# Performance work log

Measured on AMD Instinct MI355X. Metric: run time of the kernel, lower is better.

Reference implementation:

```python
import jax, jax.numpy as jnp
import numpy as np

N, E = 50000, 800000
IN_DIM, H_DIM, OUT_DIM, EDGE_DIM, HEADS = 128, 128, 112, 8, 1
NEG_SLOPE = 0.2
BN_EPS = 1e-5


def _gat_layer(x, src, dst, edge_att, W, a_src, a_dst, We, a_edge, bias):
    """PyG GATConv (concat=False, edge_dim used for attention only)."""
    H, C = a_src.shape  # heads, out channels
    xs = (x @ W).reshape(-1, H, C)            # [N,H,C]
    ef = (edge_att @ We).reshape(-1, H, C)    # [E,H,C]
    al_src = jnp.einsum('nhc,hc->nh', xs, a_src)   # [N,H]
    al_dst = jnp.einsum('nhc,hc->nh', xs, a_dst)   # [N,H]
    al_edge = jnp.einsum('ehc,hc->eh', ef, a_edge) # [E,H]
    alpha = al_src[src] + al_dst[dst] + al_edge    # [E,H]
    alpha = jnp.where(alpha > 0, alpha, NEG_SLOPE * alpha)  # leaky_relu(0.2)
    # segment softmax over incoming edges of each dst node
    m = jax.lax.stop_gradient(jax.ops.segment_max(alpha, dst, num_segments=N))
    ex = jnp.exp(alpha - m[dst])
    den = jax.ops.segment_sum(ex, dst, num_segments=N)
    att = ex / den[dst]                       # [E,H]
    msg = xs[src] * att[:, :, None]           # [E,H,C] gather + weight
    out = jax.ops.segment_sum(msg, dst, num_segments=N)  # scatter-add [N,H,C]
    return out.mean(axis=1) + bias            # concat=False -> head mean


def _batchnorm(h, gamma, beta):
    mu = h.mean(axis=0)
    var = h.var(axis=0)
    return gamma * (h - mu) * jax.lax.rsqrt(var + BN_EPS) + beta


def setup_inputs() -> dict:
    key = jax.random.key(0)
    ks = jax.random.split(key, 20)
    s = 0.1
    inp = {
        'x': jax.random.normal(ks[0], (N, IN_DIM), dtype=jnp.float32),
        'edge_index': jax.random.randint(ks[1], (2, E), 0, N, dtype=jnp.int32),
        'edge_att': jax.random.normal(ks[2], (E, EDGE_DIM), dtype=jnp.float32),
        # layer 0: IN_DIM -> H_DIM
        'W0': s * jax.random.normal(ks[3], (IN_DIM, HEADS * H_DIM), dtype=jnp.float32),
        'a_src0': s * jax.random.normal(ks[4], (HEADS, H_DIM), dtype=jnp.float32),
        'a_dst0': s * jax.random.normal(ks[5], (HEADS, H_DIM), dtype=jnp.float32),
        'We0': s * jax.random.normal(ks[6], (EDGE_DIM, HEADS * H_DIM), dtype=jnp.float32),
        'a_edge0': s * jax.random.normal(ks[7], (HEADS, H_DIM), dtype=jnp.float32),
        'b0': jnp.zeros((H_DIM,), dtype=jnp.float32),
        # layer 1: H_DIM -> OUT_DIM
        'W1': s * jax.random.normal(ks[8], (H_DIM, HEADS * OUT_DIM), dtype=jnp.float32),
        'a_src1': s * jax.random.normal(ks[9], (HEADS, OUT_DIM), dtype=jnp.float32),
        'a_dst1': s * jax.random.normal(ks[10], (HEADS, OUT_DIM), dtype=jnp.float32),
        'We1': s * jax.random.normal(ks[11], (EDGE_DIM, HEADS * OUT_DIM), dtype=jnp.float32),
        'a_edge1': s * jax.random.normal(ks[12], (HEADS, OUT_DIM), dtype=jnp.float32),
        'b1': jnp.zeros((OUT_DIM,), dtype=jnp.float32),
        # batchnorms
        'bn_g': jnp.ones((H_DIM,), dtype=jnp.float32),
        'bn_b': jnp.zeros((H_DIM,), dtype=jnp.float32),
        'bnf_g': jnp.ones((OUT_DIM,), dtype=jnp.float32),
        'bnf_b': jnp.zeros((OUT_DIM,), dtype=jnp.float32),
    }
    return inp


def reference(x, edge_index, edge_att,
              W0, a_src0, a_dst0, We0, a_edge0, b0,
              W1, a_src1, a_dst1, We1, a_edge1, b1,
              bn_g, bn_b, bnf_g, bnf_b):
    src, dst = edge_index[0], edge_index[1]
    h = _gat_layer(x, src, dst, edge_att, W0, a_src0, a_dst0, We0, a_edge0, b0)
    h = _batchnorm(h, bn_g, bn_b)
    h = jax.nn.relu(h)
    # dropout is a no-op in eval; omitted for a deterministic reference
    h = _gat_layer(h, src, dst, edge_att, W1, a_src1, a_dst1, We1, a_edge1, b1)
    h = _batchnorm(h, bnf_g, bnf_b)
    return h
```

## Files before the change

kernel.cpp:

```cpp
#include <hip/hip_runtime.h>
#include <math.h>

#define NN 50000
#define NPAD 50048
#define NE 800000
#define SCAN_B 256
#define SCAN_NBLK ((NN + SCAN_B - 1) / SCAN_B)
#define AGG_NBLK 3200

typedef __attribute__((ext_vector_type(8))) short bf16x8;
typedef __attribute__((ext_vector_type(4))) float f32x4;
typedef __attribute__((ext_vector_type(8))) unsigned short u16x8;

__device__ __forceinline__ unsigned short f2bf(float x) {
    unsigned u = __float_as_uint(x);
    u += 0x7fffu + ((u >> 16) & 1);
    return (unsigned short)(u >> 16);
}
__device__ __forceinline__ float bf2f(unsigned short h) {
    return __uint_as_float(((unsigned)h) << 16);
}

template<int LAYER>
__device__ __forceinline__ float edge_ex(uint2 r, float aldv, const float* __restrict__ als)
{
    float ae = bf2f((unsigned short)(LAYER ? (r.y & 0xffffu) : (r.x >> 16)));
    float a = als[r.x & 0xffffu] + aldv + ae;
    a = a > 0.f ? a : 0.2f * a;
    return __expf(a);
}

__global__ void k_init_cvt(int* __restrict__ deg, float* __restrict__ stats,
                           int* __restrict__ hist, int* __restrict__ binCur,
                           const float* __restrict__ We0, const float* __restrict__ ae0,
                           const float* __restrict__ We1, const float* __restrict__ ae1,
                           float* __restrict__ ve,
                           const float* __restrict__ W0, const float* __restrict__ W1,
                           unsigned short* __restrict__ Wth0, unsigned short* __restrict__ Wtl0,
                           unsigned short* __restrict__ Wth1, unsigned short* __restrict__ Wtl1)
{
    int idx = blockIdx.x * 256 + threadIdx.x;
    if (idx < NN) deg[idx] = 0;
    if (idx < 512) stats[idx] = 0.f;
    if (idx < 64) { hist[idx] = 0; binCur[idx] = 0; }
    if (idx < 128 * 128) {
        int k = idx / 128, c = idx % 128;
        float v = W0[idx];
        unsigned short hi = f2bf(v);
        Wth0[c * 128 + k] = hi;
        Wtl0[c * 128 + k] = f2bf(v - bf2f(hi));
    } else if (idx < 128 * 128 + 128 * 112) {
        int i2 = idx - 128 * 128;
        int k = i2 / 112, c = i2 % 112;
        float v = W1[i2];
        unsigned short hi = f2bf(v);
        Wth1[c * 128 + k] = hi;
        Wtl1[c * 128 + k] = f2bf(v - bf2f(hi));
    }
    if (blockIdx.x == gridDim.x - 1) {
        int j = threadIdx.x;
        if (j < 8) {
            float s = 0.f;
            for (int c = 0; c < 128; ++c) s += We0[j * 128 + c] * ae0[c];
            ve[j] = s;
        } else if (j < 16) {
            int jj = j - 8;
            float s = 0.f;
            for (int c = 0; c < 112; ++c) s += We1[jj * 112 + c] * ae1[c];
            ve[8 + jj] = s;
        }
    }
}

__global__ void k_deg(const int* __restrict__ dst, int* __restrict__ deg,
                      int* __restrict__ rank, int E_)
{
    int e = blockIdx.x * blockDim.x + threadIdx.x;
    if (e < E_) rank[e] = atomicAdd(&deg[dst[e]], 1);
}

__global__ void k_scan1(const int* __restrict__ deg, int* __restrict__ partial,
                        int* __restrict__ hist)
{
    __shared__ int sm[SCAN_B];
    __shared__ int lh[64];
    int t = threadIdx.x;
    if (t < 64) lh[t] = 0;
    int idx = blockIdx.x * SCAN_B + t;
    int d = (idx < NN) ? deg[idx] : 0;
    sm[t] = d;
    __syncthreads();
    if (idx < NN) atomicAdd(&lh[63 - (d < 63 ? d : 63)], 1);
    #pragma unroll
    for (int off = SCAN_B / 2; off > 0; off >>= 1) {
        if (t < off) sm[t] += sm[t + off];
        __syncthreads();
    }
    if (t == 0) partial[blockIdx.x] = sm[0];
    if (t < 64 && lh[t]) atomicAdd(&hist[t], lh[t]);
}

__global__ void k_scan3(const int* __restrict__ deg, const int* __restrict__ partial,
                        int* __restrict__ rp, const int* __restrict__ hist,
                        int* __restrict__ binCur, int* __restrict__ ord)
{
    __shared__ int sm[SCAN_B];
    __shared__ int pbase;
    __shared__ int lh[64], lrsv[64], lstart[64];
    int t = threadIdx.x;
    int pv = (t < SCAN_NBLK && t < blockIdx.x) ? partial[t] : 0;
    sm[t] = pv;
    __syncthreads();
    #pragma unroll
    for (int off = SCAN_B / 2; off > 0; off >>= 1) {
        if (t < off) sm[t] += sm[t + off];
        __syncthreads();
    }
    if (t == 0) pbase = sm[0];
    __syncthreads();
    int idx = blockIdx.x * SCAN_B + t;
    int v = (idx < NN) ? deg[idx] : 0;
    sm[t] = v;
    __syncthreads();
    #pragma unroll
    for (int off = 1; off < SCAN_B; off <<= 1) {
        int u = (t >= off) ? sm[t - off] : 0;
        __syncthreads();
        sm[t] += u;
        __syncthreads();
    }
    int excl = pbase + ((t == 0) ? 0 : sm[t - 1]);
    if (idx < NN) rp[idx] = excl;
    if (idx == NN - 1) rp[NN] = excl + v;

    if (t < 64) lh[t] = 0;
    __syncthreads();
    int b = 0, lr = 0;
    if (idx < NN) {
        b = 63 - (v < 63 ? v : 63);
        lr = atomicAdd(&lh[b], 1);
    }
    __syncthreads();
    if (t < 64) {
        lrsv[t] = lh[t] ? atomicAdd(&binCur[t], lh[t]) : 0;
        int s = 0;
        for (int i = 0; i < t; ++i) s += hist[i];
        lstart[t] = s;
    }
    __syncthreads();
    if (idx < NN) ord[lstart[b] + lrsv[b] + lr] = idx;
}

__global__ void k_csr_fill(const int* __restrict__ src, const int* __restrict__ dst,
                           const float* __restrict__ eatt, const float* __restrict__ ve,
                           const int* __restrict__ rp, const int* __restrict__ rank,
                           uint2* __restrict__ pk, int E_)
{
    int i = blockIdx.x * blockDim.x + threadIdx.x;
    int e = i * 2;
    if (e >= E_) return;
    int2 ss = *reinterpret_cast<const int2*>(src + e);
    int2 dd = *reinterpret_cast<const int2*>(dst + e);
    int2 rr = *reinterpret_cast<const int2*>(rank + e);
    const float4* ea = reinterpret_cast<const float4*>(eatt + (size_t)e * 8);
    float4 ea0 = ea[0], ea1 = ea[1], ea2 = ea[2], ea3 = ea[3];

    float a0x = ea0.x * ve[0] + ea0.y * ve[1] + ea0.z * ve[2] + ea0.w * ve[3]
              + ea1.x * ve[4] + ea1.y * ve[5] + ea1.z * ve[6] + ea1.w * ve[7];
    float a1x = ea0.x * ve[8] + ea0.y * ve[9] + ea0.z * ve[10] + ea0.w * ve[11]
              + ea1.x * ve[12] + ea1.y * ve[13] + ea1.z * ve[14] + ea1.w * ve[15];
    float a0y = ea2.x * ve[0] + ea2.y * ve[1] + ea2.z * ve[2] + ea2.w * ve[3]
              + ea3.x * ve[4] + ea3.y * ve[5] + ea3.z * ve[6] + ea3.w * ve[7];
    float a1y = ea2.x * ve[8] + ea2.y * ve[9] + ea2.z * ve[10] + ea2.w * ve[11]
              + ea3.x * ve[12] + ea3.y * ve[13] + ea3.z * ve[14] + ea3.w * ve[15];

    int p0 = rp[dd.x] + rr.x;
    int p1 = rp[dd.y] + rr.y;
    uint2 r0, r1;
    r0.x = (unsigned)ss.x | ((unsigned)f2bf(a0x) << 16);
    r0.y = (unsigned)f2bf(a1x);
    r1.x = (unsigned)ss.y | ((unsigned)f2bf(a0y) << 16);
    r1.y = (unsigned)f2bf(a1y);
    pk[p0] = r0;
    pk[p1] = r1;
}

template<int COLS, bool BN_IN>
__launch_bounds__(256, 2)
__global__ void k_gemm_mfma(const float* __restrict__ A,
                            const unsigned short* __restrict__ Wth,
                            const unsigned short* __restrict__ Wtl,
                            unsigned short* __restrict__ out,
                            const float* __restrict__ a_src, const float* __restrict__ a_dst,
                            float* __restrict__ als, float* __restrict__ ald,
                            const float* __restrict__ bsum, const float* __restrict__ bsq,
                            const float* __restrict__ gamma, const float* __restrict__ beta)
{
    constexpr int NT = COLS / 16;
    __shared__ unsigned short sBh[COLS * 128];
    __shared__ unsigned short sBl[COLS * 128];
    __shared__ float scN[128], shN[128];

    int wv = threadIdx.x >> 6;
    int lane = threadIdx.x & 63;
    int r0 = blockIdx.x * 64 + wv * 16;
    int m = lane & 15;
    int quad = lane >> 4;
    int arow = r0 + m;
    int rc = (arow < NN) ? arow : NN - 1;
    const float* pa = A + (size_t)rc * 128 + quad * 8;

    float4 av[8];
    #pragma unroll
    for (int ks = 0; ks < 4; ++ks) {
        av[2 * ks]     = *reinterpret_cast<const float4*>(pa + ks * 32);
        av[2 * ks + 1] = *reinterpret_cast<const float4*>(pa + ks * 32 + 4);
    }

    constexpr int CH = COLS * 128 * 2 / 16;
    for (int i = threadIdx.x; i < CH; i += 256) {
        unsigned o = (unsigned)i * 16u;
        unsigned d = o ^ (((o >> 8) & 7u) << 4);
        *reinterpret_cast<uint4*>(reinterpret_cast<char*>(sBh) + d) =
            *reinterpret_cast<const uint4*>(reinterpret_cast<const char*>(Wth) + o);
        *reinterpret_cast<uint4*>(reinterpret_cast<char*>(sBl) + d) =
            *reinterpret_cast<const uint4*>(reinterpret_cast<const char*>(Wtl) + o);
    }
    if (BN_IN) {
        if (threadIdx.x < 128) {
            int k = threadIdx.x;
            float invn = 1.0f / (float)NN;
            float mean = bsum[k] * invn;
            float var  = bsq[k] * invn - mean * mean;
            float sc = gamma[k] * rsqrtf(var + 1e-5f);
            scN[k] = sc;
            shN[k] = beta[k] - mean * sc;
        }
    }
    __syncthreads();

    f32x4 acc[NT];
    #pragma unroll
    for (int t = 0; t < NT; ++t) acc[t] = f32x4{0.f, 0.f, 0.f, 0.f};

    unsigned swz = ((unsigned)(m & 7)) << 4;

    #pragma unroll
    for (int ks = 0; ks < 4; ++ks) {
        float4 v0 = av[2 * ks], v1 = av[2 * ks + 1];
        float vv[8] = {v0.x, v0.y, v0.z, v0.w, v1.x, v1.y, v1.z, v1.w};
        int kb = ks * 32 + quad * 8;
        bf16x8 ah, al;
        #pragma unroll
        for (int jj = 0; jj < 8; ++jj) {
            float f = vv[jj];
            if (BN_IN) f = fmaxf(f * scN[kb + jj] + shN[kb + jj], 0.f);
            unsigned short hi = f2bf(f);
            ah[jj] = (short)hi;
            al[jj] = (short)f2bf(f - bf2f(hi));
        }
        #pragma unroll
        for (int t = 0; t < NT; ++t) {
            int c = t * 16 + m;
            unsigned b = ((unsigned)c * 256u + (unsigned)ks * 64u + (unsigned)quad * 16u) ^ swz;
            bf16x8 bh = *reinterpret_cast<const bf16x8*>(reinterpret_cast<const char*>(sBh) + b);
            bf16x8 bl = *reinterpret_cast<const bf16x8*>(reinterpret_cast<const char*>(sBl) + b);
            acc[t] = __builtin_amdgcn_mfma_f32_16x16x32_bf16(ah, bh, acc[t], 0, 0, 0);
            acc[t] = __builtin_amdgcn_mfma_f32_16x16x32_bf16(al, bh, acc[t], 0, 0, 0);
            acc[t] = __builtin_amdgcn_mfma_f32_16x16x32_bf16(ah, bl, acc[t], 0, 0, 0);
        }
    }

    float p[4] = {0.f, 0.f, 0.f, 0.f}, q[4] = {0.f, 0.f, 0.f, 0.f};
    #pragma unroll
    for (int t = 0; t < NT; ++t) {
        int c = t * 16 + m;
        float asv = a_src[c], adv = a_dst[c];
        #pragma unroll
        for (int rI = 0; rI < 4; ++rI) {
            float v = acc[t][rI];
            int row = r0 + quad * 4 + rI;
            if (row < NN) out[(size_t)row * COLS + c] = f2bf(v);
            p[rI] += v * asv;
            q[rI] += v * adv;
        }
    }
    #pragma unroll
    for (int rI = 0; rI < 4; ++rI) {
        #pragma unroll
        for (int off = 1; off <= 8; off <<= 1) {
            p[rI] += __shfl_xor(p[rI], off);
            q[rI] += __shfl_xor(q[rI], off);
        }
    }
    if (m == 0) {
        #pragma unroll
        for (int rI = 0; rI < 4; ++rI) {
            int row = r0 + quad * 4 + rI;
            if (row < NN) { als[row] = p[rI]; ald[row] = q[rI]; }
        }
    }
}

template<int COLS, int LAYER>
__global__ void k_aggregate(const int* __restrict__ rp, const int* __restrict__ ord,
                            const uint2* __restrict__ pk,
                            const float* __restrict__ als, const float* __restrict__ ald,
                            const unsigned short* __restrict__ xs, float* __restrict__ out,
                            float* __restrict__ psum, float* __restrict__ psq)
{
    __shared__ float sS[16 * 128], sQ[16 * 128];
    int ql = threadIdx.x & 15;
    int wq = threadIdx.x >> 4;
    int col = ql * 8;
    bool act = (col < COLS);
    int qid = blockIdx.x * 16 + wq;
    float bs[8] = {0.f,0.f,0.f,0.f,0.f,0.f,0.f,0.f};
    float bq[8] = {0.f,0.f,0.f,0.f,0.f,0.f,0.f,0.f};

    if (qid < NN) {
        int w = ord[qid];
        int beg = rp[w], end = rp[w + 1];
        float aldv = ald[w];
        float acc[8] = {0.f,0.f,0.f,0.f,0.f,0.f,0.f,0.f};
        float den = 0.f;
        int j = beg;
        for (; j + 8 <= end; j += 8) {
            uint2 r0 = pk[j],     r1 = pk[j + 1], r2 = pk[j + 2], r3 = pk[j + 3];
            uint2 r4 = pk[j + 4], r5 = pk[j + 5], r6 = pk[j + 6], r7 = pk[j + 7];
            float e0 = edge_ex<LAYER>(r0, aldv, als), e1 = edge_ex<LAYER>(r1, aldv, als);
            float e2 = edge_ex<LAYER>(r2, aldv, als), e3 = edge_ex<LAYER>(r3, aldv, als);
            float e4 = edge_ex<LAYER>(r4, aldv, als), e5 = edge_ex<LAYER>(r5, aldv, als);
            float e6 = edge_ex<LAYER>(r6, aldv, als), e7 = edge_ex<LAYER>(r7, aldv, als);
            den += ((e0 + e1) + (e2 + e3)) + ((e4 + e5) + (e6 + e7));
            if (act) {
                u16x8 u0 = *reinterpret_cast<const u16x8*>(xs + (size_t)(r0.x & 0xffffu) * COLS + col);
                u16x8 u1 = *reinterpret_cast<const u16x8*>(xs + (size_t)(r1.x & 0xffffu) * COLS + col);
                u16x8 u2 = *reinterpret_cast<const u16x8*>(xs + (size_t)(r2.x & 0xffffu) * COLS + col);
                u16x8 u3 = *reinterpret_cast<const u16x8*>(xs + (size_t)(r3.x & 0xffffu) * COLS + col);
                u16x8 u4 = *reinterpret_cast<const u16x8*>(xs + (size_t)(r4.x & 0xffffu) * COLS + col);
                u16x8 u5 = *reinterpret_cast<const u16x8*>(xs + (size_t)(r5.x & 0xffffu) * COLS + col);
                u16x8 u6 = *reinterpret_cast<const u16x8*>(xs + (size_t)(r6.x & 0xffffu) * COLS + col);
                u16x8 u7 = *reinterpret_cast<const u16x8*>(xs + (size_t)(r7.x & 0xffffu) * COLS + col);
                #pragma unroll
                for (int k = 0; k < 8; ++k)
                    acc[k] += (((e0 * bf2f(u0[k]) + e1 * bf2f(u1[k]))
                              + (e2 * bf2f(u2[k]) + e3 * bf2f(u3[k])))
                             + ((e4 * bf2f(u4[k]) + e5 * bf2f(u5[k]))
                              + (e6 * bf2f(u6[k]) + e7 * bf2f(u7[k]))));
            }
        }
        if (j < end) {
            bool v1 = j + 1 < end, v2 = j + 2 < end, v3 = j + 3 < end;
            bool v4 = j + 4 < end, v5 = j + 5 < end, v6 = j + 6 < end;
            uint2 r0 = pk[j];
            uint2 r1 = v1 ? pk[j + 1] : uint2{0u, 0u};
            uint2 r2 = v2 ? pk[j + 2] : uint2{0u, 0u};
            uint2 r3 = v3 ? pk[j + 3] : uint2{0u, 0u};
            uint2 r4 = v4 ? pk[j + 4] : uint2{0u, 0u};
            uint2 r5 = v5 ? pk[j + 5] : uint2{0u, 0u};
            uint2 r6 = v6 ? pk[j + 6] : uint2{0u, 0u};
            float e0 = edge_ex<LAYER>(r0, aldv, als);
            float e1 = v1 ? edge_ex<LAYER>(r1, aldv, als) : 0.f;
            float e2 = v2 ? edge_ex<LAYER>(r2, aldv, als) : 0.f;
            float e3 = v3 ? edge_ex<LAYER>(r3, aldv, als) : 0.f;
            float e4 = v4 ? edge_ex<LAYER>(r4, aldv, als) : 0.f;
            float e5 = v5 ? edge_ex<LAYER>(r5, aldv, als) : 0.f;
            float e6 = v6 ? edge_ex<LAYER>(r6, aldv, als) : 0.f;
            den += ((e0 + e1) + (e2 + e3)) + ((e4 + e5) + e6);
            if (act) {
                u16x8 u0 = *reinterpret_cast<const u16x8*>(xs + (size_t)(r0.x & 0xffffu) * COLS + col);
                #pragma unroll
                for (int k = 0; k < 8; ++k) acc[k] += e0 * bf2f(u0[k]);
                if (v1) {
                    u16x8 u = *reinterpret_cast<const u16x8*>(xs + (size_t)(r1.x & 0xffffu) * COLS + col);
                    #pragma unroll
                    for (int k = 0; k < 8; ++k) acc[k] += e1 * bf2f(u[k]);
                }
                if (v2) {
                    u16x8 u = *reinterpret_cast<const u16x8*>(xs + (size_t)(r2.x & 0xffffu) * COLS + col);
                    #pragma unroll
                    for (int k = 0; k < 8; ++k) acc[k] += e2 * bf2f(u[k]);
                }
                if (v3) {
                    u16x8 u = *reinterpret_cast<const u16x8*>(xs + (size_t)(r3.x & 0xffffu) * COLS + col);
                    #pragma unroll
                    for (int k = 0; k < 8; ++k) acc[k] += e3 * bf2f(u[k]);
                }
                if (v4) {
                    u16x8 u = *reinterpret_cast<const u16x8*>(xs + (size_t)(r4.x & 0xffffu) * COLS + col);
                    #pragma unroll
                    for (int k = 0; k < 8; ++k) acc[k] += e4 * bf2f(u[k]);
                }
                if (v5) {
                    u16x8 u = *reinterpret_cast<const u16x8*>(xs + (size_t)(r5.x & 0xffffu) * COLS + col);
                    #pragma unroll
                    for (int k = 0; k < 8; ++k) acc[k] += e5 * bf2f(u[k]);
                }
                if (v6) {
                    u16x8 u = *reinterpret_cast<const u16x8*>(xs + (size_t)(r6.x & 0xffffu) * COLS + col);
                    #pragma unroll
                    for (int k = 0; k < 8; ++k) acc[k] += e6 * bf2f(u[k]);
                }
            }
        }
        float inv = (end > beg) ? 1.f / den : 0.f;
        if (act) {
            float o[8];
            #pragma unroll
            for (int k = 0; k < 8; ++k) {
                o[k] = acc[k] * inv;
                bs[k] += o[k];
                bq[k] += o[k] * o[k];
            }
            f32x4 o0 = {o[0], o[1], o[2], o[3]};
            f32x4 o1 = {o[4], o[5], o[6], o[7]};
            __builtin_nontemporal_store(o0, reinterpret_cast<f32x4*>(out + (size_t)w * COLS + col));
            __builtin_nontemporal_store(o1, reinterpret_cast<f32x4*>(out + (size_t)w * COLS + col + 4));
        }
    }
    #pragma unroll
    for (int k = 0; k < 8; ++k) {
        sS[wq * 128 + col + k] = act ? bs[k] : 0.f;
        sQ[wq * 128 + col + k] = act ? bq[k] : 0.f;
    }
    __syncthreads();
    int t = threadIdx.x;
    if (t < 128) {
        float s = 0.f, s2 = 0.f;
        #pragma unroll
        for (int r = 0; r < 16; ++r) { s += sS[r * 128 + t]; s2 += sQ[r * 128 + t]; }
        psum[(size_t)blockIdx.x * 128 + t] = s;
        psq [(size_t)blockIdx.x * 128 + t] = s2;
    }
}

__global__ void k_bn_stats2(const float* __restrict__ psum, const float* __restrict__ psq,
                            float* __restrict__ sums, float* __restrict__ sqs)
{
    int t = threadIdx.x;
    int c = t & 127;
    constexpr int ROWS = AGG_NBLK / 128;
    const float* sp = (t < 128) ? psum : psq;
    float s = 0.f;
    #pragma unroll 5
    for (int i = 0; i < ROWS; ++i)
        s += sp[(size_t)(blockIdx.x * ROWS + i) * 128 + c];
    unsafeAtomicAdd(((t < 128) ? sums : sqs) + c, s);
}

template<int COLS>
__global__ void k_bn_apply(const float* __restrict__ in, float* __restrict__ out,
                           const float* __restrict__ sums, const float* __restrict__ sqs,
                           const float* __restrict__ gamma, const float* __restrict__ beta,
                           int n)
{
    int idx = blockIdx.x * blockDim.x + threadIdx.x;
    if (idx >= n * COLS) return;
    int c = idx % COLS;
    float invn = 1.0f / (float)n;
    float mean = sums[c] * invn;
    float var  = sqs[c] * invn - mean * mean;
    float sc = gamma[c] * rsqrtf(var + 1e-5f);
    float sh = beta[c] - mean * sc;
    out[idx] = in[idx] * sc + sh;
}

extern "C" void kernel_launch(void* const* d_in, const int* in_sizes, int n_in,
                              void* d_out, int out_size, void* d_ws, size_t ws_size,
                              hipStream_t stream)
{
    const float* x    = (const float*)d_in[0];
    const int*   eidx = (const int*)d_in[1];
    const float* eatt = (const float*)d_in[2];
    const float* W0   = (const float*)d_in[3];
    const float* as0  = (const float*)d_in[4];
    const float* ad0  = (const float*)d_in[5];
    const float* We0  = (const float*)d_in[6];
    const float* ae0  = (const float*)d_in[7];
    const float* W1   = (const float*)d_in[9];
    const float* as1  = (const float*)d_in[10];
    const float* ad1  = (const float*)d_in[11];
    const float* We1  = (const float*)d_in[12];
    const float* ae1  = (const float*)d_in[13];
    const float* bng  = (const float*)d_in[15];
    const float* bnb  = (const float*)d_in[16];
    const float* bnfg = (const float*)d_in[17];
    const float* bnfb = (const float*)d_in[18];

    const int N = NN, E = NE;
    const int* src = eidx;
    const int* dst = eidx + E;

    float* ws = (float*)d_ws;
    size_t off = 0;
    unsigned short* xs0b = (unsigned short*)(ws + off); off += (size_t)N * 64;
    float* h   = ws + off;      off += (size_t)N * 128;
    unsigned short* xs1b = (unsigned short*)(ws + off); off += (size_t)N * 56;
    uint2* pk = (uint2*)(ws + off);     off += (size_t)E * 2;
    int*   rp   = (int*)(ws + off);     off += N + 2;
    int*   ord  = (int*)(ws + off);     off += N;
    float* als0 = ws + off;     off += N;
    float* ald0 = ws + off;     off += N;
    float* als1 = ws + off;     off += N;
    float* ald1 = ws + off;     off += N;
    float* stats = ws + off;    off += 512;
    float* ve = ws + off;       off += 16;
    int*   hist = (int*)(ws + off);     off += 64;
    int*   binCur = (int*)(ws + off);   off += 64;
    int*   partial = (int*)(ws + off);  off += SCAN_NBLK;
    float* psum = ws + off;     off += (size_t)AGG_NBLK * 128;
    float* psq  = ws + off;     off += (size_t)AGG_NBLK * 128;
    unsigned short* Wth0 = (unsigned short*)(ws + off); off += 128 * 64;
    unsigned short* Wtl0 = (unsigned short*)(ws + off); off += 128 * 64;
    unsigned short* Wth1 = (unsigned short*)(ws + off); off += 112 * 64;
    unsigned short* Wtl1 = (unsigned short*)(ws + off); off += 112 * 64;

    int*   rank = (int*)h;
    int*   deg  = (int*)(h + 800000);
    float* out1 = h;

    float* sum0 = stats;
    float* sq0  = stats + 128;
    float* sum1 = stats + 256;
    float* sq1  = stats + 384;

    k_init_cvt<<<(N + 255) / 256, 256, 0, stream>>>(deg, stats, hist, binCur,
                                                    We0, ae0, We1, ae1, ve,
                                                    W0, W1, Wth0, Wtl0, Wth1, Wtl1);

    k_deg<<<(E + 255) / 256, 256, 0, stream>>>(dst, deg, rank, E);
    k_scan1<<<SCAN_NBLK, SCAN_B, 0, stream>>>(deg, partial, hist);
    k_scan3<<<SCAN_NBLK, SCAN_B, 0, stream>>>(deg, partial, rp, hist, binCur, ord);
    k_csr_fill<<<(E / 2 + 255) / 256, 256, 0, stream>>>(src, dst, eatt, ve, rp, rank, pk, E);

    k_gemm_mfma<128, false><<<NPAD / 64, 256, 0, stream>>>(x, Wth0, Wtl0, xs0b,
                                                           as0, ad0, als0, ald0,
                                                           nullptr, nullptr, nullptr, nullptr);
    k_aggregate<128, 0><<<AGG_NBLK, 256, 0, stream>>>(rp, ord, pk, als0, ald0, xs0b, h, psum, psq);
    k_bn_stats2<<<128, 256, 0, stream>>>(psum, psq, sum0, sq0);

    k_gemm_mfma<112, true><<<NPAD / 64, 256, 0, stream>>>(h, Wth1, Wtl1, xs1b,
                                                          as1, ad1, als1, ald1,
                                                          sum0, sq0, bng, bnb);
    k_aggregate<112, 1><<<AGG_NBLK, 256, 0, stream>>>(rp, ord, pk, als1, ald1, xs1b, out1, psum, psq);
    k_bn_stats2<<<128, 256, 0, stream>>>(psum, psq, sum1, sq1);
    k_bn_apply<112><<<(N * 112 + 255) / 256, 256, 0, stream>>>(out1, (float*)d_out, sum1, sq1, bnfg, bnfb, N);
}
```

Measured before the change: 332.4 us.

## Store aggregated activations as bf16 and widen edge-preprocessing kernels

```diff
diff --git a/kernel.cpp b/kernel.cpp
--- a/kernel.cpp
+++ b/kernel.cpp
@@ -75,8 +75,17 @@
 __global__ void k_deg(const int* __restrict__ dst, int* __restrict__ deg,
                       int* __restrict__ rank, int E_)
 {
-    int e = blockIdx.x * blockDim.x + threadIdx.x;
-    if (e < E_) rank[e] = atomicAdd(&deg[dst[e]], 1);
+    int i = blockIdx.x * blockDim.x + threadIdx.x;
+    int e = i * 2;
+    if (e + 2 <= E_) {
+        int2 dd = *reinterpret_cast<const int2*>(dst + e);
+        int2 rr;
+        rr.x = atomicAdd(&deg[dd.x], 1);
+        rr.y = atomicAdd(&deg[dd.y], 1);
+        *reinterpret_cast<int2*>(rank + e) = rr;
+    } else if (e < E_) {
+        rank[e] = atomicAdd(&deg[dst[e]], 1);
+    }
 }
 
 __global__ void k_scan1(const int* __restrict__ deg, int* __restrict__ partial,
@@ -157,37 +166,39 @@
                            uint2* __restrict__ pk, int E_)
 {
     int i = blockIdx.x * blockDim.x + threadIdx.x;
-    int e = i * 2;
+    int e = i * 4;
     if (e >= E_) return;
-    int2 ss = *reinterpret_cast<const int2*>(src + e);
-    int2 dd = *reinterpret_cast<const int2*>(dst + e);
-    int2 rr = *reinterpret_cast<const int2*>(rank + e);
+    int4 ss = *reinterpret_cast<const int4*>(src + e);
+    int4 dd = *reinterpret_cast<const int4*>(dst + e);
+    int4 rr = *reinterpret_cast<const int4*>(rank + e);
     const float4* ea = reinterpret_cast<const float4*>(eatt + (size_t)e * 8);
-    float4 ea0 = ea[0], ea1 = ea[1], ea2 = ea[2], ea3 = ea[3];
-
-    float a0x = ea0.x * ve[0] + ea0.y * ve[1] + ea0.z * ve[2] + ea0.w * ve[3]
-              + ea1.x * ve[4] + ea1.y * ve[5] + ea1.z * ve[6] + ea1.w * ve[7];
-    float a1x = ea0.x * ve[8] + ea0.y * ve[9] + ea0.z * ve[10] + ea0.w * ve[11]
-              + ea1.x * ve[12] + ea1.y * ve[13] + ea1.z * ve[14] + ea1.w * ve[15];
-    float a0y = ea2.x * ve[0] + ea2.y * ve[1] + ea2.z * ve[2] + ea2.w * ve[3]
-              + ea3.x * ve[4] + ea3.y * ve[5] + ea3.z * ve[6] + ea3.w * ve[7];
-    float a1y = ea2.x * ve[8] + ea2.y * ve[9] + ea2.z * ve[10] + ea2.w * ve[11]
-              + ea3.x * ve[12] + ea3.y * ve[13] + ea3.z * ve[14] + ea3.w * ve[15];
-
-    int p0 = rp[dd.x] + rr.x;
-    int p1 = rp[dd.y] + rr.y;
-    uint2 r0, r1;
-    r0.x = (unsigned)ss.x | ((unsigned)f2bf(a0x) << 16);
-    r0.y = (unsigned)f2bf(a1x);
-    r1.x = (unsigned)ss.y | ((unsigned)f2bf(a0y) << 16);
-    r1.y = (unsigned)f2bf(a1y);
-    pk[p0] = r0;
-    pk[p1] = r1;
+
+    float v0 = ve[0], v1 = ve[1], v2 = ve[2], v3 = ve[3];
+    float v4 = ve[4], v5 = ve[5], v6 = ve[6], v7 = ve[7];
+    float w0 = ve[8], w1 = ve[9], w2 = ve[10], w3 = ve[11];
+    float w4 = ve[12], w5 = ve[13], w6 = ve[14], w7 = ve[15];
+
+    int s4[4] = {ss.x, ss.y, ss.z, ss.w};
+    int d4[4] = {dd.x, dd.y, dd.z, dd.w};
+    int r4[4] = {rr.x, rr.y, rr.z, rr.w};
+    #pragma unroll
+    for (int k = 0; k < 4; ++k) {
+        float4 u0 = ea[2 * k], u1 = ea[2 * k + 1];
+        float a0 = u0.x * v0 + u0.y * v1 + u0.z * v2 + u0.w * v3
+                 + u1.x * v4 + u1.y * v5 + u1.z * v6 + u1.w * v7;
+        float a1 = u0.x * w0 + u0.y * w1 + u0.z * w2 + u0.w * w3
+                 + u1.x * w4 + u1.y * w5 + u1.z * w6 + u1.w * w7;
+        int pos = rp[d4[k]] + r4[k];
+        uint2 rec;
+        rec.x = (unsigned)s4[k] | ((unsigned)f2bf(a0) << 16);
+        rec.y = (unsigned)f2bf(a1);
+        pk[pos] = rec;
+    }
 }
 
 template<int COLS, bool BN_IN>
 __launch_bounds__(256, 2)
-__global__ void k_gemm_mfma(const float* __restrict__ A,
+__global__ void k_gemm_mfma(const void* __restrict__ A,
                             const unsigned short* __restrict__ Wth,
                             const unsigned short* __restrict__ Wtl,
                             unsigned short* __restrict__ out,
@@ -208,13 +219,22 @@
     int quad = lane >> 4;
     int arow = r0 + m;
     int rc = (arow < NN) ? arow : NN - 1;
-    const float* pa = A + (size_t)rc * 128 + quad * 8;
 
     float4 av[8];
-    #pragma unroll
-    for (int ks = 0; ks < 4; ++ks) {
-        av[2 * ks]     = *reinterpret_cast<const float4*>(pa + ks * 32);
-        av[2 * ks + 1] = *reinterpret_cast<const float4*>(pa + ks * 32 + 4);
+    u16x8 av16[4];
+    if (BN_IN) {
+        const unsigned short* pa = reinterpret_cast<const unsigned short*>(A)
+                                 + (size_t)rc * 128 + quad * 8;
+        #pragma unroll
+        for (int ks = 0; ks < 4; ++ks)
+            av16[ks] = *reinterpret_cast<const u16x8*>(pa + ks * 32);
+    } else {
+        const float* pa = reinterpret_cast<const float*>(A) + (size_t)rc * 128 + quad * 8;
+        #pragma unroll
+        for (int ks = 0; ks < 4; ++ks) {
+            av[2 * ks]     = *reinterpret_cast<const float4*>(pa + ks * 32);
+            av[2 * ks + 1] = *reinterpret_cast<const float4*>(pa + ks * 32 + 4);
+        }
     }
 
     constexpr int CH = COLS * 128 * 2 / 16;
@@ -247,8 +267,15 @@
 
     #pragma unroll
     for (int ks = 0; ks < 4; ++ks) {
-        float4 v0 = av[2 * ks], v1 = av[2 * ks + 1];
-        float vv[8] = {v0.x, v0.y, v0.z, v0.w, v1.x, v1.y, v1.z, v1.w};
+        float vv[8];
+        if (BN_IN) {
+            #pragma unroll
+            for (int jj = 0; jj < 8; ++jj) vv[jj] = bf2f((unsigned short)av16[ks][jj]);
+        } else {
+            float4 v0 = av[2 * ks], v1 = av[2 * ks + 1];
+            vv[0] = v0.x; vv[1] = v0.y; vv[2] = v0.z; vv[3] = v0.w;
+            vv[4] = v1.x; vv[5] = v1.y; vv[6] = v1.z; vv[7] = v1.w;
+        }
         int kb = ks * 32 + quad * 8;
         bf16x8 ah, al;
         #pragma unroll
@@ -306,7 +333,8 @@
 __global__ void k_aggregate(const int* __restrict__ rp, const int* __restrict__ ord,
                             const uint2* __restrict__ pk,
                             const float* __restrict__ als, const float* __restrict__ ald,
-                            const unsigned short* __restrict__ xs, float* __restrict__ out,
+                            const unsigned short* __restrict__ xs,
+                            unsigned short* __restrict__ out,
                             float* __restrict__ psum, float* __restrict__ psq)
 {
     __shared__ float sS[16 * 128], sQ[16 * 128];
@@ -407,16 +435,16 @@
         float inv = (end > beg) ? 1.f / den : 0.f;
         if (act) {
             float o[8];
+            u16x8 ob;
             #pragma unroll
             for (int k = 0; k < 8; ++k) {
                 o[k] = acc[k] * inv;
                 bs[k] += o[k];
                 bq[k] += o[k] * o[k];
+                ob[k] = f2bf(o[k]);
             }
-            f32x4 o0 = {o[0], o[1], o[2], o[3]};
-            f32x4 o1 = {o[4], o[5], o[6], o[7]};
-            __builtin_nontemporal_store(o0, reinterpret_cast<f32x4*>(out + (size_t)w * COLS + col));
-            __builtin_nontemporal_store(o1, reinterpret_cast<f32x4*>(out + (size_t)w * COLS + col + 4));
+            __builtin_nontemporal_store(ob,
+                reinterpret_cast<u16x8*>(out + (size_t)w * COLS + col));
         }
     }
     #pragma unroll
@@ -450,7 +478,7 @@
 }
 
 template<int COLS>
-__global__ void k_bn_apply(const float* __restrict__ in, float* __restrict__ out,
+__global__ void k_bn_apply(const unsigned short* __restrict__ in, float* __restrict__ out,
                            const float* __restrict__ sums, const float* __restrict__ sqs,
                            const float* __restrict__ gamma, const float* __restrict__ beta,
                            int n)
@@ -463,7 +491,7 @@
     float var  = sqs[c] * invn - mean * mean;
     float sc = gamma[c] * rsqrtf(var + 1e-5f);
     float sh = beta[c] - mean * sc;
-    out[idx] = in[idx] * sc + sh;
+    out[idx] = bf2f(in[idx]) * sc + sh;
 }
 
 extern "C" void kernel_launch(void* const* d_in, const int* in_sizes, int n_in,
@@ -495,7 +523,7 @@
     float* ws = (float*)d_ws;
     size_t off = 0;
     unsigned short* xs0b = (unsigned short*)(ws + off); off += (size_t)N * 64;
-    float* h   = ws + off;      off += (size_t)N * 128;
+    unsigned short* h = (unsigned short*)(ws + off);    off += (size_t)N * 64;
     unsigned short* xs1b = (unsigned short*)(ws + off); off += (size_t)N * 56;
     uint2* pk = (uint2*)(ws + off);     off += (size_t)E * 2;
     int*   rp   = (int*)(ws + off);     off += N + 2;
@@ -517,8 +545,8 @@
     unsigned short* Wtl1 = (unsigned short*)(ws + off); off += 112 * 64;
 
     int*   rank = (int*)h;
-    int*   deg  = (int*)(h + 800000);
-    float* out1 = h;
+    int*   deg  = ((int*)h) + 800000;
+    unsigned short* out1 = h;
 
     float* sum0 = stats;
     float* sq0  = stats + 128;
@@ -529,10 +557,10 @@
                                                     We0, ae0, We1, ae1, ve,
                                                     W0, W1, Wth0, Wtl0, Wth1, Wtl1);
 
-    k_deg<<<(E + 255) / 256, 256, 0, stream>>>(dst, deg, rank, E);
+    k_deg<<<(E / 2 + 255) / 256, 256, 0, stream>>>(dst, deg, rank, E);
     k_scan1<<<SCAN_NBLK, SCAN_B, 0, stream>>>(deg, partial, hist);
     k_scan3<<<SCAN_NBLK, SCAN_B, 0, stream>>>(deg, partial, rp, hist, binCur, ord);
-    k_csr_fill<<<(E / 2 + 255) / 256, 256, 0, stream>>>(src, dst, eatt, ve, rp, rank, pk, E);
+    k_csr_fill<<<(E / 4 + 255) / 256, 256, 0, stream>>>(src, dst, eatt, ve, rp, rank, pk, E);
 
     k_gemm_mfma<128, false><<<NPAD / 64, 256, 0, stream>>>(x, Wth0, Wtl0, xs0b,
                                                            as0, ad0, als0, ald0,
```

After: 329.4 us. Within noise of the previous version (-0.9%).
